# Kernel tuning notes

Hardware: AMD Instinct MI355X
Metric: run time of the kernel (lower is better)

## Reference

```python
import jax, jax.numpy as jnp
import numpy as np

SEQ_LEN = 131072
NUM_NODES = 256
NUM_CAUSES = 16
NUM_FEATURES = 100
NUM_OUTPUTS = 1
NOISE_STD = 0.01


def _build_dag_mask(N, C, p, rng):
    # upper-triangular random adjacency; roots (0..C-1) have no parents;
    # every non-root gets at least one parent (mirrors _build_random_dag)
    A = (rng.random((N, N)) < p) & np.triu(np.ones((N, N), bool), k=1)
    A[:, :C] = False
    for j in range(C, N):
        if not A[:j, j].any():
            A[rng.integers(0, j), j] = True
    return A.astype(np.int32)


def setup_inputs() -> dict:
    key = jax.random.key(0)
    k1, k2, k3 = jax.random.split(key, 3)
    rng = np.random.default_rng(0)
    S, N, C = SEQ_LEN, NUM_NODES, NUM_CAUSES
    causes = jax.random.normal(k1, (S, C), dtype=jnp.float32)
    W = jax.random.normal(k2, (N, N), dtype=jnp.float32)  # edge weights w_ij ~ N(0,1)
    eps = jax.random.normal(k3, (S, N - C), dtype=jnp.float32)  # unit noise, scaled by NOISE_STD
    mask = jnp.asarray(_build_dag_mask(N, C, 0.3, rng))
    act_id = jnp.asarray(rng.integers(0, 4, size=(N - C,)), dtype=jnp.int32)
    # y from a sink-like last node; X from sorted sample of remaining non-root nodes
    y_idx = jnp.asarray([N - 1], dtype=jnp.int64)
    X_idx = jnp.asarray(np.sort(rng.choice(np.arange(C, N - 1), size=NUM_FEATURES, replace=False)), dtype=jnp.int64)
    return {"causes": causes, "W": W, "eps": eps, "mask": mask, "act_id": act_id, "X_idx": X_idx, "y_idx": y_idx}


def reference(causes, W, eps, mask, act_id, X_idx, y_idx):
    S, C = causes.shape
    N = W.shape[0]
    Wm = W * mask.astype(W.dtype)                      # [N,N] masked edge weights (parent i -> node j)
    vals0 = jnp.zeros((S, N), W.dtype).at[:, :C].set(causes)
    Wcols = Wm.T[C:]                                   # [N-C, N] incoming-weight rows per non-root node
    eps_t = eps.T                                      # [N-C, S]
    branches = [lambda z: z, jnp.tanh, jax.nn.relu, jax.nn.sigmoid]

    def step(carry, xs):
        vals, idx = carry
        w_col, e, a = xs
        z = vals @ w_col + jnp.float32(NOISE_STD) * e  # weighted parent sum + noise, [S]
        v = jax.lax.switch(a, branches, z)
        vals = vals.at[:, idx].set(v)
        return (vals, idx + 1), None

    (vals, _), _ = jax.lax.scan(step, (vals0, jnp.int32(C)), (Wcols, eps_t, act_id))
    X = vals[:, X_idx]                                 # [S, num_features]
    y = vals[:, y_idx]                                 # [S, 1]
    bad = jnp.isnan(X).any() | jnp.isnan(y).any()
    X = jnp.where(bad, jnp.float32(0.0), X)
    y = jnp.where(bad, jnp.float32(-100.0), y)
    return X, y[:, 0]                                  # num_outputs == 1 -> squeeze
```

## Files before the change

### kernel.cpp

```cpp
#include <hip/hip_runtime.h>
#include <hip/hip_bf16.h>
#include <hip/hip_fp16.h>


typedef _Float16 half8 __attribute__((ext_vector_type(8)));
typedef float    f32x4 __attribute__((ext_vector_type(4)));

constexpr int S_LEN    = 131072;
constexpr int N_NODES  = 256;
constexpr int N_CAUSES = 16;
constexpr int N_COMP   = 240;
constexpr int N_FEAT   = 100;
constexpr float NOISE  = 0.01f;
constexpr float VSC    = 0.0625f;
constexpr float VSCI   = 16.0f;

constexpr int KE_tab[16]  = {0,32,64,64,96,96,128,128,160,160,192,192,224,224,256,256};
constexpr int OFF_tab[16] = {0,0,1024,3072,5120,8192,11264,15360,19456,24576,29696,
                             35840,41984,49152,56320,64512};

__constant__ int c_KE[16]  = {0,32,64,64,96,96,128,128,160,160,192,192,224,224,256,256};
__constant__ int c_OFF[16] = {0,0,1024,3072,5120,8192,11264,15360,19456,24576,29696,
                              35840,41984,49152,56320,64512};

__device__ _Float16 g_WT[72704];
__device__ float    g_Wtri[15 * 256];

__device__ __forceinline__ bool sniff_binary64(const void* p) {
    const unsigned* u = (const unsigned*)p;
    bool ok = true;
    for (int i = 0; i < 64; ++i) ok = ok && (u[i] <= 1u);
    return ok;
}
__device__ __forceinline__ bool sniff_is_bf16(const void* p) {
    const unsigned* u = (const unsigned*)p;
    bool ok = true;
    for (int i = 0; i < 16; ++i) {
        unsigned e = ((u[i] << 16) >> 23) & 0xffu;
        ok = ok && (e >= 100u) && (e <= 132u);
    }
    return ok;
}
__device__ __forceinline__ float bflo(unsigned u) { return __uint_as_float(u << 16); }
__device__ __forceinline__ float bfhi(unsigned u) { return __uint_as_float(u & 0xffff0000u); }

__device__ __forceinline__ void load16(const void* base, long long off, bool isbf, float* o) {
    if (isbf) {
        const uint4* p = (const uint4*)((const unsigned short*)base + off);
        uint4 a = p[0], b = p[1];
        o[0]=bflo(a.x); o[1]=bfhi(a.x); o[2]=bflo(a.y); o[3]=bfhi(a.y);
        o[4]=bflo(a.z); o[5]=bfhi(a.z); o[6]=bflo(a.w); o[7]=bfhi(a.w);
        o[8]=bflo(b.x); o[9]=bfhi(b.x); o[10]=bflo(b.y); o[11]=bfhi(b.y);
        o[12]=bflo(b.z); o[13]=bfhi(b.z); o[14]=bflo(b.w); o[15]=bfhi(b.w);
    } else {
        const float4* p = (const float4*)((const float*)base + off);
        float4 x0=p[0], x1=p[1], x2=p[2], x3=p[3];
        o[0]=x0.x; o[1]=x0.y; o[2]=x0.z; o[3]=x0.w;
        o[4]=x1.x; o[5]=x1.y; o[6]=x1.z; o[7]=x1.w;
        o[8]=x2.x; o[9]=x2.y; o[10]=x2.z; o[11]=x2.w;
        o[12]=x3.x; o[13]=x3.y; o[14]=x3.z; o[15]=x3.w;
    }
}

__device__ __forceinline__ float hw_exp2(float x) {
    float r; asm("v_exp_f32 %0, %1" : "=v"(r) : "v"(x)); return r;
}
__device__ __forceinline__ float hw_rcp(float x) {
    float r; asm("v_rcp_f32 %0, %1" : "=v"(r) : "v"(x)); return r;
}
__device__ __forceinline__ float fast_tanh(float x) {
    float t = hw_exp2(x * 2.88539008177792681f);
    return 1.0f - 2.0f * hw_rcp(t + 1.0f);
}
__device__ __forceinline__ float fast_sigmoid(float x) {
    return hw_rcp(1.0f + hw_exp2(x * -1.44269504088896341f));
}

__global__ void prep_kernel(const void* __restrict__ A, const void* __restrict__ B) {
    __shared__ int s_mA, s_wbf;
    if (threadIdx.x == 0) {
        s_mA  = sniff_binary64(A) ? 1 : 0;
        s_wbf = sniff_is_bf16(s_mA ? B : A) ? 1 : 0;
    }
    __syncthreads();
    const int*  maskp = (const int*)(s_mA ? A : B);
    const void* Wp    = s_mA ? B : A;
    const int k = blockIdx.x + 1, j0 = 16 * k, KE = c_KE[k], OFF = c_OFF[k];
    const int tid = threadIdx.x;

    for (int n = 0; n < 16; ++n) {
        const int j = j0 + n;
        for (int kk = tid; kk < KE; kk += 256) {
            const int gi = kk * N_NODES + j;
            float w = 0.0f;
            if (maskp[gi])
                w = s_wbf ? __bfloat162float(((const __hip_bfloat16*)Wp)[gi])
                          : ((const float*)Wp)[gi];
            const _Float16 hi = (_Float16)w;
            const _Float16 lo = (_Float16)(w - (float)hi);
            g_WT[OFF + n * KE + kk]           = hi;
            g_WT[OFF + 16 * KE + n * KE + kk] = lo;
        }
    }
    {
        const int l = tid >> 4, i = tid & 15;
        const int gi = (j0 + l) * N_NODES + (j0 + i);
        float w = 0.0f;
        if (l < i && maskp[gi])
            w = s_wbf ? __bfloat162float(((const __hip_bfloat16*)Wp)[gi])
                      : ((const float*)Wp)[gi];
        g_Wtri[(k - 1) * 256 + tid] = w;
    }
}

#define MFMA16(a, b, c) __builtin_amdgcn_mfma_f32_16x16x32_f16((a), (b), (c), 0, 0, 0)

template<int K>
__device__ __forceinline__ void do_chunk(
    const int lane, const long long sg,
    const void* __restrict__ eps, const bool ebf,
    half8 (&vf)[4][8],
    float* __restrict__ Zbuf, _Float16* __restrict__ stag,
    const short* __restrict__ xpos, const int* __restrict__ act_id,
    float* __restrict__ wsX,
    float* __restrict__ outX, float* __restrict__ outY, const int yi)
{
    constexpr int j0  = 16 * K;
    constexpr int KE  = KE_tab[K];
    constexpr int NST = KE / 32;
    constexpr int OFF = OFF_tab[K];

    const int mrow = lane & 15;
    const int quad = lane >> 4;

    float ev[16];
    load16(eps, sg * (long long)N_COMP + (j0 - N_CAUSES), ebf, ev);

    const _Float16* __restrict__ bp = g_WT + OFF + mrow * KE + (quad << 3);

    f32x4 acc0 = {0.f,0.f,0.f,0.f}, acc1 = {0.f,0.f,0.f,0.f};
    f32x4 acc2 = {0.f,0.f,0.f,0.f}, acc3 = {0.f,0.f,0.f,0.f};

    #pragma unroll
    for (int t = 0; t < NST; ++t) {
        const half8 bh = *(const half8*)(bp + (t << 5));
        const half8 bl = *(const half8*)(bp + 16 * KE + (t << 5));
        acc0 = MFMA16(vf[0][t], bh, acc0);
        acc1 = MFMA16(vf[1][t], bh, acc1);
        acc2 = MFMA16(vf[2][t], bh, acc2);
        acc3 = MFMA16(vf[3][t], bh, acc3);
        acc0 = MFMA16(vf[0][t], bl, acc0);
        acc1 = MFMA16(vf[1][t], bl, acc1);
        acc2 = MFMA16(vf[2][t], bl, acc2);
        acc3 = MFMA16(vf[3][t], bl, acc3);
    }

    {
        const int r0 = quad << 2;
        #pragma unroll
        for (int r = 0; r < 4; ++r) {
            Zbuf[(r0 + r)      * 21 + mrow] = acc0[r] * VSCI;
            Zbuf[(16 + r0 + r) * 21 + mrow] = acc1[r] * VSCI;
            Zbuf[(32 + r0 + r) * 21 + mrow] = acc2[r] * VSCI;
            Zbuf[(48 + r0 + r) * 21 + mrow] = acc3[r] * VSCI;
        }
    }
    __builtin_amdgcn_wave_barrier();

    float zz[16];
    #pragma unroll
    for (int i = 0; i < 16; ++i) zz[i] = Zbuf[lane * 21 + i];

    const float* __restrict__ tri = g_Wtri + (K - 1) * 256;
    float vn[16];
    half8 h0, h1;
    #pragma unroll
    for (int i = 0; i < 16; ++i) {
        float z = zz[i] + NOISE * ev[i];
        #pragma unroll
        for (int l = 0; l < i; ++l) z += tri[(l << 4) + i] * vn[l];
        const int a = act_id[j0 - N_CAUSES + i];
        if (a == 1)      z = fast_tanh(z);
        else if (a == 2) z = fmaxf(z, 0.0f);
        else if (a == 3) z = fast_sigmoid(z);
        vn[i] = z;
        if (i < 8) h0[i] = (_Float16)(z * VSC);
        else       h1[i - 8] = (_Float16)(z * VSC);
        const int xp = xpos[j0 - N_CAUSES + i];
        if (xp >= 0) {
            if (wsX) wsX[(long long)xp * S_LEN + sg] = z;
            else     outX[xp] = z;
        }
        if (j0 + i == yi) outY[sg] = z;
    }

    *(half8*)(stag + lane * 24)     = h0;
    *(half8*)(stag + lane * 24 + 8) = h1;
    __builtin_amdgcn_wave_barrier();

    constexpr int TT = K >> 1;
    constexpr int HB = (K & 1) << 1;
    const int hq = lane >> 4;
    if (hq == HB || hq == HB + 1) {
        const int boff = (hq - HB) << 3;
        #pragma unroll
        for (int q = 0; q < 4; ++q)
            vf[q][TT] = *(const half8*)(stag + (q * 16 + (lane & 15)) * 24 + boff);
    }
    __builtin_amdgcn_wave_barrier();
}

__global__ __launch_bounds__(64, 2)
void scm_kernel(const void* __restrict__ causes,
                const void* __restrict__ eps,
                const int* __restrict__ act_id,
                const void* __restrict__ xidx_raw,
                const int* __restrict__ yidx_raw,
                float* __restrict__ out,
                float* __restrict__ wsX,
                long long ybase) {
    __shared__ __align__(16) float    Zbuf[64 * 21];
    __shared__ __align__(16) _Float16 stag[64 * 24];
    __shared__ short xpos[N_COMP];

    const int lane = threadIdx.x;
    const long long sg = (long long)blockIdx.x * 64 + lane;

    for (int t = lane; t < N_COMP; t += 64) xpos[t] = -1;
    const unsigned long long* x64 = (const unsigned long long*)xidx_raw;
    const int*                x32 = (const int*)xidx_raw;
    const bool is64 = ((x64[0] >> 32) == 0ull);
    __builtin_amdgcn_wave_barrier();
    for (int f = lane; f < N_FEAT; f += 64) {
        const int ix = is64 ? (int)x64[f] : x32[f];
        xpos[ix - N_CAUSES] = (short)f;
    }
    __builtin_amdgcn_wave_barrier();
    const int yi  = yidx_raw[0];
    const bool cbf = sniff_is_bf16(causes);
    const bool ebf = sniff_is_bf16(eps);

    half8 vz;
    #pragma unroll
    for (int e = 0; e < 8; ++e) vz[e] = (_Float16)0.0f;
    half8 vf[4][8];
    #pragma unroll
    for (int q = 0; q < 4; ++q) {
        #pragma unroll
        for (int t = 0; t < 8; ++t) vf[q][t] = vz;
    }

    {
        float cv[16];
        load16(causes, sg * (long long)N_CAUSES, cbf, cv);
        half8 c0, c1;
        #pragma unroll
        for (int i = 0; i < 8; ++i) {
            c0[i] = (_Float16)(cv[i] * VSC);
            c1[i] = (_Float16)(cv[8 + i] * VSC);
        }
        *(half8*)(stag + lane * 24)     = c0;
        *(half8*)(stag + lane * 24 + 8) = c1;
        __builtin_amdgcn_wave_barrier();
        const int hq = lane >> 4;
        if (hq < 2) {
            #pragma unroll
            for (int q = 0; q < 4; ++q)
                vf[q][0] = *(const half8*)(stag + (q * 16 + (lane & 15)) * 24 + (hq << 3));
        }
        __builtin_amdgcn_wave_barrier();
    }

    float* outX = out + sg * N_FEAT;
    float* outY = out + ybase;

    do_chunk< 1>(lane, sg, eps, ebf, vf, Zbuf, stag, xpos, act_id, wsX, outX, outY, yi);
    do_chunk< 2>(lane, sg, eps, ebf, vf, Zbuf, stag, xpos, act_id, wsX, outX, outY, yi);
    do_chunk< 3>(lane, sg, eps, ebf, vf, Zbuf, stag, xpos, act_id, wsX, outX, outY, yi);
    do_chunk< 4>(lane, sg, eps, ebf, vf, Zbuf, stag, xpos, act_id, wsX, outX, outY, yi);
    do_chunk< 5>(lane, sg, eps, ebf, vf, Zbuf, stag, xpos, act_id, wsX, outX, outY, yi);
    do_chunk< 6>(lane, sg, eps, ebf, vf, Zbuf, stag, xpos, act_id, wsX, outX, outY, yi);
    do_chunk< 7>(lane, sg, eps, ebf, vf, Zbuf, stag, xpos, act_id, wsX, outX, outY, yi);
    do_chunk< 8>(lane, sg, eps, ebf, vf, Zbuf, stag, xpos, act_id, wsX, outX, outY, yi);
    do_chunk< 9>(lane, sg, eps, ebf, vf, Zbuf, stag, xpos, act_id, wsX, outX, outY, yi);
    do_chunk<10>(lane, sg, eps, ebf, vf, Zbuf, stag, xpos, act_id, wsX, outX, outY, yi);
    do_chunk<11>(lane, sg, eps, ebf, vf, Zbuf, stag, xpos, act_id, wsX, outX, outY, yi);
    do_chunk<12>(lane, sg, eps, ebf, vf, Zbuf, stag, xpos, act_id, wsX, outX, outY, yi);
    do_chunk<13>(lane, sg, eps, ebf, vf, Zbuf, stag, xpos, act_id, wsX, outX, outY, yi);
    do_chunk<14>(lane, sg, eps, ebf, vf, Zbuf, stag, xpos, act_id, wsX, outX, outY, yi);
    do_chunk<15>(lane, sg, eps, ebf, vf, Zbuf, stag, xpos, act_id, wsX, outX, outY, yi);
}

__global__ __launch_bounds__(256)
void xpose_kernel(const float* __restrict__ ws, float* __restrict__ out) {
    __shared__ float tile[64 * 100];
    const int tid = threadIdx.x;
    const long long s0 = (long long)blockIdx.x * 64;
    const int f = tid >> 6;
    const int s = tid & 63;
    #pragma unroll
    for (int g = 0; g < 25; ++g) {
        const int ff = f + g * 4;
        tile[s * 100 + ff] = ws[(long long)ff * S_LEN + s0 + s];
    }
    __syncthreads();
    float4* o4 = (float4*)(out + s0 * N_FEAT);
    const float4* t4 = (const float4*)tile;
    #pragma unroll
    for (int g = 0; g < 7; ++g) {
        const int idx = g * 256 + tid;
        if (idx < 1600) o4[idx] = t4[idx];
    }
}

extern "C" void kernel_launch(void* const* d_in, const int* in_sizes, int n_in,
                              void* d_out, int out_size, void* d_ws, size_t ws_size,
                              hipStream_t stream) {
    int ic = 0, iw = 1, ie = 2, im = 3, ia = 4, ix = 5, iy = 6;
    int c = -1, e = -1, a = -1, x = -1, y = -1, m1 = -1, m2 = -1;
    for (int i = 0; i < n_in; ++i) {
        switch (in_sizes[i]) {
            case S_LEN * N_CAUSES:   c = i; break;
            case S_LEN * N_COMP:     e = i; break;
            case N_COMP:             a = i; break;
            case N_FEAT:             x = i; break;
            case 1:                  y = i; break;
            case N_NODES * N_NODES:  (m1 < 0 ? m1 : m2) = i; break;
        }
    }
    if (c >= 0 && e >= 0 && a >= 0 && x >= 0 && y >= 0 && m1 >= 0 && m2 >= 0) {
        ic = c; ie = e; ia = a; ix = x; iy = y; iw = m1; im = m2;
    }

    const void* causes = d_in[ic];
    const void* TA     = d_in[iw];
    const void* TB     = d_in[im];
    const void* eps    = d_in[ie];
    const int*  act_id = (const int*)d_in[ia];
    const void* xidx   = d_in[ix];
    const int*  yidx   = (const int*)d_in[iy];
    float*      out    = (float*)d_out;
    const long long ybase = (long long)out_size - S_LEN;

    const bool usews = ws_size >= (size_t)N_FEAT * S_LEN * sizeof(float);
    float* wsX = usews ? (float*)d_ws : nullptr;

    prep_kernel<<<15, 256, 0, stream>>>(TA, TB);
    scm_kernel<<<S_LEN / 64, 64, 0, stream>>>(causes, eps, act_id, xidx, yidx,
                                              out, wsX, ybase);
    if (usews)
        xpose_kernel<<<S_LEN / 64, 256, 0, stream>>>(wsX, out);
}
```

Before: 356.0 us.

## Halve samples per wave, split MFMA accumulators, use push-style triangular solve

Each 64-lane wave now handles 32 samples instead of 64. Each sample still runs on one lane for the serial per-chunk work, so lanes 32-63 only help with the MFMA fragments. The MFMA chain is split into separate high and low accumulators to shorten the dependency chain, and the in-chunk triangular recurrence is reordered into a forward-push update that keeps fewer live registers. Occupancy bounds go from 2 to 4 waves and the grid doubles. This trades half-idle lanes in the scalar epilogue for more waves in flight and lower register pressure, which helps hide latency.

```diff
diff --git a/kernel.cpp b/kernel.cpp
--- a/kernel.cpp
+++ b/kernel.cpp
@@ -119,7 +119,7 @@
 __device__ __forceinline__ void do_chunk(
     const int lane, const long long sg,
     const void* __restrict__ eps, const bool ebf,
-    half8 (&vf)[4][8],
+    half8 (&vf)[2][8],
     float* __restrict__ Zbuf, _Float16* __restrict__ stag,
     const short* __restrict__ xpos, const int* __restrict__ act_id,
     float* __restrict__ wsX,
@@ -134,68 +134,64 @@
     const int quad = lane >> 4;
 
     float ev[16];
-    load16(eps, sg * (long long)N_COMP + (j0 - N_CAUSES), ebf, ev);
+    if (lane < 32)
+        load16(eps, sg * (long long)N_COMP + (j0 - N_CAUSES), ebf, ev);
 
     const _Float16* __restrict__ bp = g_WT + OFF + mrow * KE + (quad << 3);
 
-    f32x4 acc0 = {0.f,0.f,0.f,0.f}, acc1 = {0.f,0.f,0.f,0.f};
-    f32x4 acc2 = {0.f,0.f,0.f,0.f}, acc3 = {0.f,0.f,0.f,0.f};
+    f32x4 acc0h = {0.f,0.f,0.f,0.f}, acc0l = {0.f,0.f,0.f,0.f};
+    f32x4 acc1h = {0.f,0.f,0.f,0.f}, acc1l = {0.f,0.f,0.f,0.f};
 
     #pragma unroll
     for (int t = 0; t < NST; ++t) {
         const half8 bh = *(const half8*)(bp + (t << 5));
         const half8 bl = *(const half8*)(bp + 16 * KE + (t << 5));
-        acc0 = MFMA16(vf[0][t], bh, acc0);
-        acc1 = MFMA16(vf[1][t], bh, acc1);
-        acc2 = MFMA16(vf[2][t], bh, acc2);
-        acc3 = MFMA16(vf[3][t], bh, acc3);
-        acc0 = MFMA16(vf[0][t], bl, acc0);
-        acc1 = MFMA16(vf[1][t], bl, acc1);
-        acc2 = MFMA16(vf[2][t], bl, acc2);
-        acc3 = MFMA16(vf[3][t], bl, acc3);
+        acc0h = MFMA16(vf[0][t], bh, acc0h);
+        acc1h = MFMA16(vf[1][t], bh, acc1h);
+        acc0l = MFMA16(vf[0][t], bl, acc0l);
+        acc1l = MFMA16(vf[1][t], bl, acc1l);
     }
 
     {
         const int r0 = quad << 2;
         #pragma unroll
         for (int r = 0; r < 4; ++r) {
-            Zbuf[(r0 + r)      * 21 + mrow] = acc0[r] * VSCI;
-            Zbuf[(16 + r0 + r) * 21 + mrow] = acc1[r] * VSCI;
-            Zbuf[(32 + r0 + r) * 21 + mrow] = acc2[r] * VSCI;
-            Zbuf[(48 + r0 + r) * 21 + mrow] = acc3[r] * VSCI;
-        }
-    }
-    __builtin_amdgcn_wave_barrier();
-
-    float zz[16];
-    #pragma unroll
-    for (int i = 0; i < 16; ++i) zz[i] = Zbuf[lane * 21 + i];
-
-    const float* __restrict__ tri = g_Wtri + (K - 1) * 256;
-    float vn[16];
-    half8 h0, h1;
-    #pragma unroll
-    for (int i = 0; i < 16; ++i) {
-        float z = zz[i] + NOISE * ev[i];
-        #pragma unroll
-        for (int l = 0; l < i; ++l) z += tri[(l << 4) + i] * vn[l];
-        const int a = act_id[j0 - N_CAUSES + i];
-        if (a == 1)      z = fast_tanh(z);
-        else if (a == 2) z = fmaxf(z, 0.0f);
-        else if (a == 3) z = fast_sigmoid(z);
-        vn[i] = z;
-        if (i < 8) h0[i] = (_Float16)(z * VSC);
-        else       h1[i - 8] = (_Float16)(z * VSC);
-        const int xp = xpos[j0 - N_CAUSES + i];
-        if (xp >= 0) {
-            if (wsX) wsX[(long long)xp * S_LEN + sg] = z;
-            else     outX[xp] = z;
-        }
-        if (j0 + i == yi) outY[sg] = z;
-    }
-
-    *(half8*)(stag + lane * 24)     = h0;
-    *(half8*)(stag + lane * 24 + 8) = h1;
+            Zbuf[(r0 + r)      * 21 + mrow] = (acc0h[r] + acc0l[r]) * VSCI;
+            Zbuf[(16 + r0 + r) * 21 + mrow] = (acc1h[r] + acc1l[r]) * VSCI;
+        }
+    }
+    __builtin_amdgcn_wave_barrier();
+
+    if (lane < 32) {
+        float zz[16];
+        #pragma unroll
+        for (int i = 0; i < 16; ++i)
+            zz[i] = Zbuf[lane * 21 + i] + NOISE * ev[i];
+
+        const float* __restrict__ tri = g_Wtri + (K - 1) * 256;
+        half8 h0, h1;
+        #pragma unroll
+        for (int i = 0; i < 16; ++i) {
+            float z = zz[i];
+            const int a = act_id[j0 - N_CAUSES + i];
+            if (a == 1)      z = fast_tanh(z);
+            else if (a == 2) z = fmaxf(z, 0.0f);
+            else if (a == 3) z = fast_sigmoid(z);
+            if (i < 8) h0[i] = (_Float16)(z * VSC);
+            else       h1[i - 8] = (_Float16)(z * VSC);
+            const int xp = xpos[j0 - N_CAUSES + i];
+            if (xp >= 0) {
+                if (wsX) wsX[(long long)xp * S_LEN + sg] = z;
+                else     outX[xp] = z;
+            }
+            if (j0 + i == yi) outY[sg] = z;
+            #pragma unroll
+            for (int j = i + 1; j < 16; ++j)
+                zz[j] += tri[(i << 4) + j] * z;
+        }
+        *(half8*)(stag + lane * 24)     = h0;
+        *(half8*)(stag + lane * 24 + 8) = h1;
+    }
     __builtin_amdgcn_wave_barrier();
 
     constexpr int TT = K >> 1;
@@ -204,13 +200,13 @@
     if (hq == HB || hq == HB + 1) {
         const int boff = (hq - HB) << 3;
         #pragma unroll
-        for (int q = 0; q < 4; ++q)
+        for (int q = 0; q < 2; ++q)
             vf[q][TT] = *(const half8*)(stag + (q * 16 + (lane & 15)) * 24 + boff);
     }
     __builtin_amdgcn_wave_barrier();
 }
 
-__global__ __launch_bounds__(64, 2)
+__global__ __launch_bounds__(64, 4)
 void scm_kernel(const void* __restrict__ causes,
                 const void* __restrict__ eps,
                 const int* __restrict__ act_id,
@@ -219,12 +215,12 @@
                 float* __restrict__ out,
                 float* __restrict__ wsX,
                 long long ybase) {
-    __shared__ __align__(16) float    Zbuf[64 * 21];
-    __shared__ __align__(16) _Float16 stag[64 * 24];
+    __shared__ __align__(16) float    Zbuf[32 * 21];
+    __shared__ __align__(16) _Float16 stag[32 * 24];
     __shared__ short xpos[N_COMP];
 
     const int lane = threadIdx.x;
-    const long long sg = (long long)blockIdx.x * 64 + lane;
+    const long long sg = (long long)blockIdx.x * 32 + lane;
 
     for (int t = lane; t < N_COMP; t += 64) xpos[t] = -1;
     const unsigned long long* x64 = (const unsigned long long*)xidx_raw;
@@ -243,14 +239,14 @@
     half8 vz;
     #pragma unroll
     for (int e = 0; e < 8; ++e) vz[e] = (_Float16)0.0f;
-    half8 vf[4][8];
-    #pragma unroll
-    for (int q = 0; q < 4; ++q) {
+    half8 vf[2][8];
+    #pragma unroll
+    for (int q = 0; q < 2; ++q) {
         #pragma unroll
         for (int t = 0; t < 8; ++t) vf[q][t] = vz;
     }
 
-    {
+    if (lane < 32) {
         float cv[16];
         load16(causes, sg * (long long)N_CAUSES, cbf, cv);
         half8 c0, c1;
@@ -261,15 +257,17 @@
         }
         *(half8*)(stag + lane * 24)     = c0;
         *(half8*)(stag + lane * 24 + 8) = c1;
-        __builtin_amdgcn_wave_barrier();
+    }
+    __builtin_amdgcn_wave_barrier();
+    {
         const int hq = lane >> 4;
         if (hq < 2) {
             #pragma unroll
-            for (int q = 0; q < 4; ++q)
+            for (int q = 0; q < 2; ++q)
                 vf[q][0] = *(const half8*)(stag + (q * 16 + (lane & 15)) * 24 + (hq << 3));
         }
-        __builtin_amdgcn_wave_barrier();
-    }
+    }
+    __builtin_amdgcn_wave_barrier();
 
     float* outX = out + sg * N_FEAT;
     float* outY = out + ybase;
@@ -346,7 +344,7 @@
     float* wsX = usews ? (float*)d_ws : nullptr;
 
     prep_kernel<<<15, 256, 0, stream>>>(TA, TB);
-    scm_kernel<<<S_LEN / 64, 64, 0, stream>>>(causes, eps, act_id, xidx, yidx,
+    scm_kernel<<<S_LEN / 32, 64, 0, stream>>>(causes, eps, act_id, xidx, yidx,
                                               out, wsX, ybase);
     if (usews)
         xpose_kernel<<<S_LEN / 64, 256, 0, stream>>>(wsX, out);
```

Result: no change. 353.4 us (-0.7%).
